# Optimization experiments

Measured on AMD Instinct MI355X. Metric: run time of the kernel, lower is better.

## Reference

```python
import jax, jax.numpy as jnp
import numpy as np
import math

H = 2048          # hidden_size
NH = 16           # num_attn_heads
HD = H // NH      # attn head dim = 128
NFW = 4           # num_lact_heads
FD = H // NFW     # fw head dim = 512
DH = FD           # inter_multi = 1.0
CHUNK = 512       # lact_chunk_size
WINDOW = 2048     # window_size
ROPE_BASE = 500000.0
BASE_LR_INV = math.log(math.expm1(0.001))  # inv_softplus(1e-3)


def rmsnorm(x, w, eps=1e-6):
    return x * jax.lax.rsqrt(jnp.mean(x * x, axis=-1, keepdims=True) + eps) * w


def l2norm(x, eps=1e-12):
    return x * jax.lax.rsqrt(jnp.sum(x * x, axis=-1, keepdims=True) + eps)


def rope(x):  # x: [b, h, s, d], half-split convention
    d = x.shape[-1]
    s = x.shape[2]
    inv = 1.0 / (ROPE_BASE ** (jnp.arange(d // 2, dtype=jnp.float32) / (d // 2)))
    f = jnp.arange(s, dtype=jnp.float32)[:, None] * inv[None, :]  # [s, d/2]
    cos, sin = jnp.cos(f), jnp.sin(f)
    x1, x2 = x[..., : d // 2], x[..., d // 2:]
    return jnp.concatenate([x1 * cos - x2 * sin, x2 * cos + x1 * sin], axis=-1)


def setup_inputs() -> dict:
    key = jax.random.key(0)
    ks = jax.random.split(key, 8)
    b, s = 2, 2048
    return {
        "hidden_states": jax.random.normal(ks[0], (b, s, H), jnp.float32),
        "qkv_w": jax.random.normal(ks[1], (3 * H, H), jnp.float32) / math.sqrt(H),
        "q_norm_w": jnp.ones((H,), jnp.float32),
        "k_norm_w": jnp.ones((H,), jnp.float32),
        "qk_scale": jnp.ones((H, 2), jnp.float32),
        "qk_offset": jnp.zeros((H, 2), jnp.float32),
        "lr_w": jax.random.normal(ks[2], (3 * NFW, H), jnp.float32) / math.sqrt(H),
        "lr_b": jnp.zeros((3 * NFW,), jnp.float32),
        "w0": jax.random.normal(ks[3], (NFW, DH, FD), jnp.float32) / math.sqrt(FD),
        "w1": jax.random.normal(ks[4], (NFW, FD, DH), jnp.float32) / math.sqrt(DH),
        "w2": jax.random.normal(ks[5], (NFW, DH, FD), jnp.float32) / math.sqrt(FD),
        "ttt_norm_w": jnp.ones((FD,), jnp.float32),
        "o_proj_w": jax.random.normal(ks[6], (H, H), jnp.float32) / math.sqrt(H),
    }


def reference(hidden_states, qkv_w, q_norm_w, k_norm_w, qk_scale, qk_offset,
              lr_w, lr_b, w0, w1, w2, ttt_norm_w, o_proj_w):
    x = hidden_states
    b, s, _ = x.shape
    nc = s // CHUNK

    qkv = x @ qkv_w.T
    q, k, v = jnp.split(qkv, 3, axis=-1)
    q = rmsnorm(q, q_norm_w)
    k = rmsnorm(k, k_norm_w)

    # ---- TTT (fast-weight SwiGLU) branch ----
    fq = jax.nn.silu(q * qk_scale[:, 0] + qk_offset[:, 0])
    fk = jax.nn.silu(k * qk_scale[:, 1] + qk_offset[:, 1])
    fv = jax.nn.silu(v)
    tohead = lambda t: t.reshape(b, s, NFW, FD).transpose(0, 2, 1, 3)  # [b,h,s,d]
    fq, fk, fv = l2norm(tohead(fq)), l2norm(tohead(fk)), tohead(fv)

    lr = jax.nn.softplus(x @ lr_w.T + lr_b + BASE_LR_INV)          # [b,s,3*NFW]
    lr = lr.reshape(b, s, 3, NFW).transpose(2, 0, 3, 1)[..., None]  # [3,b,h,s,1]
    lr0, lr1, lr2 = lr[0], lr[1], lr[2]

    chunkify = lambda t: t.reshape(b, NFW, nc, CHUNK, -1).transpose(2, 0, 1, 3, 4)
    qs, ks_, vs = chunkify(fq), chunkify(fk), chunkify(fv)
    l0s, l1s, l2s = chunkify(lr0), chunkify(lr1), chunkify(lr2)

    w0b = jnp.broadcast_to(w0, (b,) + w0.shape)
    w1b = jnp.broadcast_to(w1, (b,) + w1.shape)
    w2b = jnp.broadcast_to(w2, (b,) + w2.shape)

    def step(carry, xs):
        w0c, w1c, w2c = carry
        qc, kc, vc, l0, l1, l2 = xs
        # apply current fast weights to queries (strictly causal across chunks)
        hq = jax.nn.silu(jnp.einsum('bhcd,bhed->bhce', qc, w0c)) * \
             jnp.einsum('bhcd,bhed->bhce', qc, w2c)
        oc = jnp.einsum('bhce,bhde->bhcd', hq, w1c)
        # gradient-descent update on dot-product loss -sum(v * f(k))
        g1 = jnp.einsum('bhcd,bhed->bhce', kc, w0c)
        g2 = jnp.einsum('bhcd,bhed->bhce', kc, w2c)
        gate = jax.nn.silu(g1)
        hidden = gate * g2
        dhidden = jnp.einsum('bhcd,bhde->bhce', vc, w1c)  # w1^T v
        dh2 = dhidden * gate
        sig = jax.nn.sigmoid(g1)
        dh1 = dhidden * g2 * (sig * (1.0 + g1 * (1.0 - sig)))  # silu'(g1)
        w1n = w1c + jnp.einsum('bhcd,bhce->bhde', l1 * vc, hidden)
        w0n = w0c + jnp.einsum('bhce,bhcd->bhed', l0 * dh1, kc)
        w2n = w2c + jnp.einsum('bhce,bhcd->bhed', l2 * dh2, kc)
        return (w0n, w1n, w2n), oc

    _, o_chunks = jax.lax.scan(step, (w0b, w1b, w2b), (qs, ks_, vs, l0s, l1s, l2s))
    o_ttt = o_chunks.transpose(1, 2, 0, 3, 4).reshape(b, NFW, s, FD)
    o_ttt = rmsnorm(o_ttt, ttt_norm_w)
    o_ttt = o_ttt.transpose(0, 2, 1, 3).reshape(b, s, H)

    # ---- sliding-window attention branch ----
    qa = rope(q.reshape(b, s, NH, HD).transpose(0, 2, 1, 3))
    ka = rope(k.reshape(b, s, NH, HD).transpose(0, 2, 1, 3))
    va = v.reshape(b, s, NH, HD).transpose(0, 2, 1, 3)
    scores = jnp.einsum('bhqd,bhkd->bhqk', qa, ka) / math.sqrt(HD)
    i = jnp.arange(s)
    mask = (i[:, None] >= i[None, :]) & (i[:, None] - i[None, :] < WINDOW)
    scores = jnp.where(mask, scores, jnp.float32(-1e9))
    p = jax.nn.softmax(scores, axis=-1)
    attn = jnp.einsum('bhqk,bhkd->bhqd', p, va).transpose(0, 2, 1, 3).reshape(b, s, H)

    return (attn + o_ttt) @ o_proj_w.T
```

## Files before the change

### kernel.cpp

```cpp
#include <hip/hip_runtime.h>
#include <hip/hip_bf16.h>
#include <math.h>

using bf16 = __hip_bfloat16;

namespace {

constexpr int cH = 2048;
constexpr int cNH = 16;
constexpr int cHD = 128;
constexpr int cNFW = 4;
constexpr int cFD = 512;
constexpr int cS = 2048;
constexpr float cRSQRT_HD = 0.08838834764831845f;
constexpr long ZL_ = 262144;
constexpr long ZG_ = 1048576;

typedef __attribute__((ext_vector_type(8))) short short8;
typedef __attribute__((ext_vector_type(4))) float f32x4;

__device__ __forceinline__ float sigmoidf_(float x) { return 1.0f / (1.0f + __expf(-x)); }
__device__ __forceinline__ float b2f(bf16 v) { return __bfloat162float(v); }
__device__ __forceinline__ bf16 f2b(float v) { return __float2bfloat16(v); }
__device__ __forceinline__ unsigned short f2bu(float f) {
  return __builtin_bit_cast(unsigned short, __float2bfloat16(f));
}

#if defined(__has_builtin)
#if __has_builtin(__builtin_amdgcn_global_load_lds)
#define HAVE_GLOAD 1
#endif
#endif

__device__ __forceinline__ void gload16(const bf16* g, short* ldsbase) {
#ifdef HAVE_GLOAD
  __builtin_amdgcn_global_load_lds((const __attribute__((address_space(1))) void*)g,
                                   (__attribute__((address_space(3))) void*)ldsbase, 16, 0, 0);
#else
  const int l = threadIdx.x & 63;
  *(uint4*)(ldsbase + l * 8) = *(const uint4*)g;
#endif
}

__device__ __forceinline__ void stage16(const bf16* src, short* dst) {
  *(uint4*)dst = *(const uint4*)src;
  *(uint4*)(dst + 8) = *(const uint4*)(src + 8);
}

__device__ __forceinline__ void store1(float* p, float v) { *p = v; }
__device__ __forceinline__ void store1(bf16* p, float v) { *p = f2b(v); }

template <int AMODE, int BMODE>
__device__ __forceinline__ void mm_core(const bf16* __restrict__ Ab, int lda,
                                        const bf16* __restrict__ Bb, int ldb, int K,
                                        const float* __restrict__ sc,
                                        short* As, short* Bs, f32x4 acc[4][4]) {
  const int t = threadIdx.x, lane = t & 63, g = lane >> 4, c16 = lane & 15;
  const int wv = t >> 6, wm = (wv >> 1) * 64, wn = (wv & 1) * 64;
  for (int k0 = 0; k0 < K; k0 += 32) {
    __syncthreads();
    if constexpr (AMODE == 0) {
      const int ch = wv * 2;
      const bf16* g0 = Ab + (size_t)(ch * 16 + (lane >> 2)) * lda + k0 + (lane & 3) * 8;
      gload16(g0, &As[ch * 512]);
      gload16(g0 + (size_t)16 * lda, &As[ch * 512 + 512]);
    } else {
      const int kk = t >> 3, mseg = (t & 7) * 16;
      const float s = sc[k0 + kk];
      const bf16* p = Ab + (size_t)(k0 + kk) * lda + mseg;
#pragma unroll
      for (int i = 0; i < 16; ++i) As[(mseg + i) * 32 + kk] = (short)f2bu(b2f(p[i]) * s);
    }
    if constexpr (BMODE == 0) {
      const int ch = wv * 2;
      const bf16* g0 = Bb + (size_t)(ch * 16 + (lane >> 2)) * ldb + k0 + (lane & 3) * 8;
      gload16(g0, &Bs[ch * 512]);
      gload16(g0 + (size_t)16 * ldb, &Bs[ch * 512 + 512]);
    } else {
      const int kk = t >> 3, cseg = (t & 7) * 16;
      const short* p = (const short*)(Bb + (size_t)(k0 + kk) * ldb + cseg);
#pragma unroll
      for (int i = 0; i < 16; ++i) Bs[(cseg + i) * 32 + kk] = p[i];
    }
    __syncthreads();
    short8 af[4], bfr[4];
#pragma unroll
    for (int mi = 0; mi < 4; ++mi) af[mi] = *(const short8*)&As[(wm + mi * 16 + c16) * 32 + g * 8];
#pragma unroll
    for (int ni = 0; ni < 4; ++ni) bfr[ni] = *(const short8*)&Bs[(wn + ni * 16 + c16) * 32 + g * 8];
#pragma unroll
    for (int mi = 0; mi < 4; ++mi)
#pragma unroll
      for (int ni = 0; ni < 4; ++ni)
        acc[mi][ni] = __builtin_amdgcn_mfma_f32_16x16x32_bf16(af[mi], bfr[ni], acc[mi][ni], 0, 0, 0);
  }
}

template <bool ACC, bool MIR, typename TC>
__device__ __forceinline__ void mm_store(TC* Cb, bf16* Mb, int ldc, int rb, int cb, f32x4 acc[4][4]) {
  const int t = threadIdx.x, lane = t & 63, g = lane >> 4, c16 = lane & 15;
  const int wv = t >> 6, wm = (wv >> 1) * 64, wn = (wv & 1) * 64;
  const int rbase = rb + wm, cbase = cb + wn;
#pragma unroll
  for (int mi = 0; mi < 4; ++mi)
#pragma unroll
    for (int ni = 0; ni < 4; ++ni) {
      const int col = cbase + ni * 16 + c16;
#pragma unroll
      for (int r = 0; r < 4; ++r) {
        const int row = rbase + mi * 16 + g * 4 + r;
        TC* cp = Cb + (size_t)row * ldc + col;
        if constexpr (ACC) {
          float nv = *cp + acc[mi][ni][r];
          *cp = nv;
          if constexpr (MIR) Mb[(size_t)row * ldc + col] = f2b(nv);
        } else {
          store1(cp, acc[mi][ni][r]);
        }
      }
    }
}

template <typename TC, int BMODE>
__global__ __launch_bounds__(256) void k_mm(const bf16* __restrict__ A, int lda, long zsa,
                                            const bf16* __restrict__ B, int ldb, long zsb,
                                            TC* __restrict__ C, int ldc, long zsc, int K) {
  __shared__ short As[128 * 32];
  __shared__ short Bs[128 * 32];
  const int z = blockIdx.z;
  const bf16* Ab = A + (size_t)z * zsa + (size_t)blockIdx.y * 128 * lda;
  const bf16* Bb = (BMODE == 0) ? (B + (size_t)z * zsb + (size_t)blockIdx.x * 128 * ldb)
                                : (B + (size_t)z * zsb + blockIdx.x * 128);
  f32x4 acc[4][4];
  const f32x4 zero4 = {0.f, 0.f, 0.f, 0.f};
#pragma unroll
  for (int i = 0; i < 4; ++i)
#pragma unroll
    for (int j = 0; j < 4; ++j) acc[i][j] = zero4;
  mm_core<0, BMODE>(Ab, lda, Bb, ldb, K, nullptr, As, Bs, acc);
  mm_store<false, false>(C + (size_t)z * zsc, (bf16*)nullptr, ldc, blockIdx.y * 128, blockIdx.x * 128, acc);
}

__global__ __launch_bounds__(256) void k_fuse1(const bf16* __restrict__ fq, const bf16* __restrict__ fk,
                                               const bf16* __restrict__ fv,
                                               const bf16* __restrict__ w0b, const bf16* __restrict__ w1bc,
                                               const bf16* __restrict__ w2b,
                                               bf16* __restrict__ hq, bf16* __restrict__ trH,
                                               bf16* __restrict__ trD1, bf16* __restrict__ trD2,
                                               bf16* __restrict__ trK, bf16* __restrict__ trV,
                                               const float* __restrict__ lr0, const float* __restrict__ lr1,
                                               const float* __restrict__ lr2,
                                               const bf16* __restrict__ occPrev,
                                               const float* __restrict__ tw, bf16* __restrict__ y,
                                               int chunk) {
  __shared__ short S[12288];
  __shared__ float red[4];
  const int id = blockIdx.x, t = threadIdx.x;
  const size_t choff = (size_t)chunk * 262144;

  if (id < 512) {
    const int bh = id >> 6, tile = id & 63, by = tile >> 3, bx = tile & 7;
    const int lane = t & 63, g = lane >> 4, c16 = lane & 15, wv = t >> 6;
    const int wm = (wv >> 1) * 32, wn = (wv & 1) * 32;
    const bf16* Aq = fq + (size_t)bh * ZG_ + choff + (size_t)(by * 64) * cFD;
    const bf16* Ak = fk + (size_t)bh * ZG_ + choff + (size_t)(by * 64) * cFD;
    const bf16* Av = fv + (size_t)bh * ZG_ + choff + (size_t)(by * 64) * cFD;
    const bf16* B0 = w0b + (size_t)bh * ZL_ + (size_t)(bx * 64) * cFD;
    const bf16* B2 = w2b + (size_t)bh * ZL_ + (size_t)(bx * 64) * cFD;
    const bf16* B1 = w1bc + (size_t)bh * ZL_ + bx * 64;

    f32x4 acc[5][2][2];
    const f32x4 zero4 = {0.f, 0.f, 0.f, 0.f};
#pragma unroll
    for (int v = 0; v < 5; ++v)
#pragma unroll
      for (int i = 0; i < 2; ++i)
#pragma unroll
        for (int j = 0; j < 2; ++j) acc[v][i][j] = zero4;

    const int srow = wv * 16 + (lane >> 2), scol = (lane & 3) * 8;
    for (int k0 = 0; k0 < 512; k0 += 32) {
      __syncthreads();
      gload16(Aq + (size_t)srow * cFD + k0 + scol, &S[0 + wv * 512]);
      gload16(Ak + (size_t)srow * cFD + k0 + scol, &S[2048 + wv * 512]);
      gload16(Av + (size_t)srow * cFD + k0 + scol, &S[4096 + wv * 512]);
      gload16(B0 + (size_t)srow * cFD + k0 + scol, &S[6144 + wv * 512]);
      gload16(B2 + (size_t)srow * cFD + k0 + scol, &S[8192 + wv * 512]);
      {
        const int kk = t >> 3, e8 = (t & 7) * 8;
        const short* p = (const short*)(B1 + (size_t)(k0 + kk) * cFD + e8);
#pragma unroll
        for (int i = 0; i < 8; ++i) S[10240 + (e8 + i) * 32 + kk] = p[i];
      }
      __syncthreads();
      short8 aq[2], ak[2], av[2], b0[2], b2[2], b1[2];
#pragma unroll
      for (int mi = 0; mi < 2; ++mi) {
        const int ro = (wm + mi * 16 + c16) * 32 + g * 8;
        aq[mi] = *(const short8*)&S[0 + ro];
        ak[mi] = *(const short8*)&S[2048 + ro];
        av[mi] = *(const short8*)&S[4096 + ro];
      }
#pragma unroll
      for (int ni = 0; ni < 2; ++ni) {
        const int ro = (wn + ni * 16 + c16) * 32 + g * 8;
        b0[ni] = *(const short8*)&S[6144 + ro];
        b2[ni] = *(const short8*)&S[8192 + ro];
        b1[ni] = *(const short8*)&S[10240 + ro];
      }
#pragma unroll
      for (int mi = 0; mi < 2; ++mi)
#pragma unroll
        for (int ni = 0; ni < 2; ++ni) {
          acc[0][mi][ni] = __builtin_amdgcn_mfma_f32_16x16x32_bf16(aq[mi], b0[ni], acc[0][mi][ni], 0, 0, 0);
          acc[1][mi][ni] = __builtin_amdgcn_mfma_f32_16x16x32_bf16(aq[mi], b2[ni], acc[1][mi][ni], 0, 0, 0);
          acc[2][mi][ni] = __builtin_amdgcn_mfma_f32_16x16x32_bf16(ak[mi], b0[ni], acc[2][mi][ni], 0, 0, 0);
          acc[3][mi][ni] = __builtin_amdgcn_mfma_f32_16x16x32_bf16(ak[mi], b2[ni], acc[3][mi][ni], 0, 0, 0);
          acc[4][mi][ni] = __builtin_amdgcn_mfma_f32_16x16x32_bf16(av[mi], b1[ni], acc[4][mi][ni], 0, 0, 0);
        }
    }

    float l0v[2][4], l2v[2][4];
#pragma unroll
    for (int mi = 0; mi < 2; ++mi)
#pragma unroll
      for (int r = 0; r < 4; ++r) {
        const int row = by * 64 + wm + mi * 16 + g * 4 + r;
        l0v[mi][r] = lr0[bh * 2048 + chunk * 512 + row];
        l2v[mi][r] = lr2[bh * 2048 + chunk * 512 + row];
      }
#pragma unroll
    for (int mi = 0; mi < 2; ++mi)
#pragma unroll
      for (int ni = 0; ni < 2; ++ni)
#pragma unroll
        for (int r = 0; r < 4; ++r) {
          float hq1 = acc[0][mi][ni][r], hq2 = acc[1][mi][ni][r];
          float g1 = acc[2][mi][ni][r], g2 = acc[3][mi][ni][r], dh = acc[4][mi][ni][r];
          acc[0][mi][ni][r] = hq1 * sigmoidf_(hq1) * hq2;
          float sg = sigmoidf_(g1);
          float gate = g1 * sg;
          acc[1][mi][ni][r] = gate * g2;
          acc[2][mi][ni][r] = l0v[mi][r] * dh * g2 * (sg * (1.0f + g1 * (1.0f - sg)));
          acc[3][mi][ni][r] = l2v[mi][r] * dh * gate;
        }

    short* Ts = S;
    bf16* dst0 = hq + (size_t)bh * ZL_;
    bf16* dstT[3] = {trH + (size_t)bh * ZL_, trD1 + (size_t)bh * ZL_, trD2 + (size_t)bh * ZL_};
#pragma unroll
    for (int rd = 0; rd < 4; ++rd) {
      __syncthreads();
#pragma unroll
      for (int mi = 0; mi < 2; ++mi)
#pragma unroll
        for (int ni = 0; ni < 2; ++ni)
#pragma unroll
          for (int r = 0; r < 4; ++r) {
            const int row = wm + mi * 16 + g * 4 + r, col = wn + ni * 16 + c16;
            if (rd == 0) Ts[row * 66 + col] = (short)f2bu(acc[0][mi][ni][r]);
            else Ts[col * 66 + row] = (short)f2bu(acc[rd][mi][ni][r]);
          }
      __syncthreads();
      const int rr = t >> 2, cs = (t & 3) * 16;
      unsigned short u[16] __attribute__((aligned(16)));
#pragma unroll
      for (int i = 0; i < 16; ++i) u[i] = (unsigned short)Ts[rr * 66 + cs + i];
      bf16* dp = (rd == 0) ? (dst0 + (size_t)(by * 64 + rr) * cFD + bx * 64 + cs)
                           : (dstT[rd - 1] + (size_t)(bx * 64 + rr) * cFD + by * 64 + cs);
      *(uint4*)dp = *(uint4*)u;
      *(uint4*)(dp + 8) = *(uint4*)(u + 8);
    }
  } else if (id < 1536) {
    short* Ts = S;
    const int id2 = id - 512;
    const int var = id2 >> 9, bh = (id2 >> 6) & 7, by = (id2 >> 3) & 7, bx = id2 & 7;
    const bf16* src = ((var == 0) ? fk : fv) + choff + (size_t)bh * ZG_;
    bf16* dst = ((var == 0) ? trK : trV) + (size_t)bh * ZL_;
    {
      const int rr = t >> 2, cseg = (t & 3) * 16;
      if (var == 0) {
        stage16(src + (size_t)(by * 64 + rr) * cFD + bx * 64 + cseg, &Ts[rr * 72 + cseg]);
      } else {
        const float s = lr1[bh * 2048 + chunk * 512 + by * 64 + rr];
        const bf16* p = src + (size_t)(by * 64 + rr) * cFD + bx * 64 + cseg;
        unsigned short u[16] __attribute__((aligned(16)));
#pragma unroll
        for (int i = 0; i < 16; ++i) u[i] = f2bu(b2f(p[i]) * s);
        *(uint4*)&Ts[rr * 72 + cseg] = *(uint4*)u;
        *(uint4*)&Ts[rr * 72 + cseg + 8] = *(uint4*)(u + 8);
      }
    }
    __syncthreads();
    {
      const int oc_ = t >> 2, rseg = (t & 3) * 16;
      unsigned short u[16] __attribute__((aligned(16)));
#pragma unroll
      for (int i = 0; i < 16; ++i) u[i] = (unsigned short)Ts[(rseg + i) * 72 + oc_];
      bf16* dp = dst + (size_t)(bx * 64 + oc_) * cFD + by * 64 + rseg;
      *(uint4*)dp = *(uint4*)u;
      *(uint4*)(dp + 8) = *(uint4*)(u + 8);
    }
  } else {
    const int rrow = id - 1536;
    const int bh = rrow >> 9, rr = rrow & 511;
    const bf16* src = occPrev + ((size_t)bh * 512 + rr) * 512;
    float v0 = b2f(src[t]), v1 = b2f(src[t + 256]);
    float ss = v0 * v0 + v1 * v1;
    for (int d = 32; d; d >>= 1) ss += __shfl_down(ss, d);
    if ((t & 63) == 0) red[t >> 6] = ss;
    __syncthreads();
    const float rstd = rsqrtf((red[0] + red[1] + red[2] + red[3]) / cFD + 1e-6f);
    const int si = (chunk - 1) * 512 + rr;
    bf16* dst = y + ((size_t)((bh >> 2) * cS) + si) * cH + (bh & 3) * cFD;
    dst[t] = f2b(b2f(dst[t]) + v0 * rstd * tw[t]);
    dst[t + 256] = f2b(b2f(dst[t + 256]) + v1 * rstd * tw[t + 256]);
  }
}

__global__ __launch_bounds__(256) void k_updna(const bf16* __restrict__ trV, const bf16* __restrict__ trH,
                                               const bf16* __restrict__ trD1, const bf16* __restrict__ trD2,
                                               const bf16* __restrict__ trK,
                                               const bf16* __restrict__ hq, const bf16* __restrict__ w1bc,
                                               float* w0s, float* w1s, float* w2s,
                                               bf16* w0b, bf16* w1bn, bf16* w2b,
                                               bf16* __restrict__ occCur) {
  __shared__ short Sh[8192];
  const int id = blockIdx.x, t = threadIdx.x;
  if (id < 384) {
    short* As = Sh;
    short* Bs = Sh + 4096;
    const int z = id >> 4, tile = id & 15, by = tile >> 2, bx = tile & 3;
    const int var = z >> 3, bh = z & 7;
    const bf16 *Aa, *Bb;
    float* W;
    bf16* M;
    if (var == 0) {
      Aa = trV + (size_t)bh * ZL_ + (size_t)by * 128 * cFD;
      Bb = trH + (size_t)bh * ZL_ + (size_t)bx * 128 * cFD;
      W = w1s + (size_t)bh * ZL_; M = w1bn + (size_t)bh * ZL_;
    } else if (var == 1) {
      Aa = trD1 + (size_t)bh * ZL_ + (size_t)by * 128 * cFD;
      Bb = trK + (size_t)bh * ZL_ + (size_t)bx * 128 * cFD;
      W = w0s + (size_t)bh * ZL_; M = w0b + (size_t)bh * ZL_;
    } else {
      Aa = trD2 + (size_t)bh * ZL_ + (size_t)by * 128 * cFD;
      Bb = trK + (size_t)bh * ZL_ + (size_t)bx * 128 * cFD;
      W = w2s + (size_t)bh * ZL_; M = w2b + (size_t)bh * ZL_;
    }
    f32x4 acc[4][4];
    const f32x4 zero4 = {0.f, 0.f, 0.f, 0.f};
#pragma unroll
    for (int i = 0; i < 4; ++i)
#pragma unroll
      for (int j = 0; j < 4; ++j) acc[i][j] = zero4;
    mm_core<0, 0>(Aa, cFD, Bb, cFD, cFD, nullptr, As, Bs, acc);
    mm_store<true, true>(W, M, cFD, by * 128, bx * 128, acc);
  } else {
    const int id2 = id - 384;
    const int bh = id2 >> 6, tile = id2 & 63, by = tile >> 3, bx = tile & 7;
    const int lane = t & 63, g = lane >> 4, c16 = lane & 15, wv = t >> 6;
    const int wm = (wv >> 1) * 32, wn = (wv & 1) * 32;
    const bf16* Aa = hq + (size_t)bh * ZL_ + (size_t)(by * 64) * cFD;
    const bf16* Bb = w1bc + (size_t)bh * ZL_ + (size_t)(bx * 64) * cFD;
    short* As = Sh;
    short* Bs = Sh + 2048;
    f32x4 acc[2][2];
    const f32x4 zero4 = {0.f, 0.f, 0.f, 0.f};
#pragma unroll
    for (int i = 0; i < 2; ++i)
#pragma unroll
      for (int j = 0; j < 2; ++j) acc[i][j] = zero4;
    for (int k0 = 0; k0 < 512; k0 += 32) {
      __syncthreads();
      {
        const int srow = wv * 16 + (lane >> 2), scol = (lane & 3) * 8;
        gload16(Aa + (size_t)srow * cFD + k0 + scol, &As[wv * 512]);
        gload16(Bb + (size_t)srow * cFD + k0 + scol, &Bs[wv * 512]);
      }
      __syncthreads();
      short8 af[2], bfr[2];
#pragma unroll
      for (int mi = 0; mi < 2; ++mi) af[mi] = *(const short8*)&As[(wm + mi * 16 + c16) * 32 + g * 8];
#pragma unroll
      for (int ni = 0; ni < 2; ++ni) bfr[ni] = *(const short8*)&Bs[(wn + ni * 16 + c16) * 32 + g * 8];
#pragma unroll
      for (int mi = 0; mi < 2; ++mi)
#pragma unroll
        for (int ni = 0; ni < 2; ++ni)
          acc[mi][ni] = __builtin_amdgcn_mfma_f32_16x16x32_bf16(af[mi], bfr[ni], acc[mi][ni], 0, 0, 0);
    }
    bf16* C = occCur + (size_t)bh * ZL_;
#pragma unroll
    for (int mi = 0; mi < 2; ++mi)
#pragma unroll
      for (int ni = 0; ni < 2; ++ni) {
        const int col = bx * 64 + wn + ni * 16 + c16;
#pragma unroll
        for (int r = 0; r < 4; ++r) {
          const int row = by * 64 + wm + mi * 16 + g * 4 + r;
          C[(size_t)row * cFD + col] = f2b(acc[mi][ni][r]);
        }
      }
  }
}

__global__ __launch_bounds__(256) void k_norm(const bf16* __restrict__ occ,
                                              const float* __restrict__ tw, bf16* __restrict__ y,
                                              int chunk) {
  __shared__ float red[4];
  const int rrow = blockIdx.x;
  const int bh = rrow >> 9, rr = rrow & 511;
  const int t = threadIdx.x;
  const bf16* src = occ + ((size_t)bh * 512 + rr) * 512;
  float v0 = b2f(src[t]), v1 = b2f(src[t + 256]);
  float ss = v0 * v0 + v1 * v1;
  for (int d = 32; d; d >>= 1) ss += __shfl_down(ss, d);
  if ((t & 63) == 0) red[t >> 6] = ss;
  __syncthreads();
  const float rstd = rsqrtf((red[0] + red[1] + red[2] + red[3]) / cFD + 1e-6f);
  const int si = chunk * 512 + rr;
  bf16* dst = y + ((size_t)((bh >> 2) * cS) + si) * cH + (bh & 3) * cFD;
  dst[t] = f2b(b2f(dst[t]) + v0 * rstd * tw[t]);
  dst[t + 256] = f2b(b2f(dst[t + 256]) + v1 * rstd * tw[t + 256]);
}

__global__ __launch_bounds__(256) void k_cvt(const float* __restrict__ src, bf16* __restrict__ dst) {
  const size_t i = ((size_t)blockIdx.x * 256 + threadIdx.x) * 8;
  float4 a = *(const float4*)(src + i), b = *(const float4*)(src + i + 4);
  unsigned short u[8] __attribute__((aligned(16)));
  u[0] = f2bu(a.x); u[1] = f2bu(a.y); u[2] = f2bu(a.z); u[3] = f2bu(a.w);
  u[4] = f2bu(b.x); u[5] = f2bu(b.y); u[6] = f2bu(b.z); u[7] = f2bu(b.w);
  *(uint4*)(dst + i) = *(uint4*)u;
}

__global__ __launch_bounds__(256) void k_winit(const float* __restrict__ w0, const float* __restrict__ w1,
                                               const float* __restrict__ w2,
                                               float* __restrict__ w0s, float* __restrict__ w1s,
                                               float* __restrict__ w2s) {
  const size_t i = (size_t)blockIdx.x * 256 + threadIdx.x;
  const int bh = (int)(i >> 18);
  const int f = bh & 3;
  const size_t off = i & 262143;
  const float* src; float* dst;
  if (blockIdx.y == 0) { src = w0; dst = w0s; }
  else if (blockIdx.y == 1) { src = w1; dst = w1s; }
  else { src = w2; dst = w2s; }
  dst[i] = src[(size_t)f * 262144 + off];
}

__global__ __launch_bounds__(64) void k_rope_tab(float* __restrict__ ct, float* __restrict__ stb) {
  const int si = blockIdx.x, j = threadIdx.x;
  float inv = powf(500000.0f, -(float)j / 64.0f);
  float ang = (float)si * inv;
  ct[(size_t)si * 64 + j] = cosf(ang);
  stb[(size_t)si * 64 + j] = sinf(ang);
}

__global__ __launch_bounds__(256) void k_lr(const float* __restrict__ x, const float* __restrict__ lr_w,
                                            const float* __restrict__ lr_b,
                                            float* lr0, float* lr1, float* lr2, float base) {
  const int token = blockIdx.x, b_ = token >> 11, si = token & 2047;
  const int wv = threadIdx.x >> 6, lane = threadIdx.x & 63;
  const float* xr = x + (size_t)token * cH;
#pragma unroll
  for (int jj = 0; jj < 3; ++jj) {
    const int j = wv * 3 + jj;
    const float* wr = lr_w + (size_t)j * cH;
    float s = 0.f;
    for (int k = lane; k < cH; k += 64) s += xr[k] * wr[k];
    for (int d = 32; d; d >>= 1) s += __shfl_down(s, d);
    if (lane == 0) {
      float v = s + lr_b[j] + base;
      float sp = (v > 15.f) ? v : log1pf(expf(v));
      const int tt = j >> 2, f = j & 3;
      float* dst = (tt == 0 ? lr0 : tt == 1 ? lr1 : lr2);
      dst[(size_t)(b_ * cNFW + f) * cS + si] = sp;
    }
  }
}

__global__ __launch_bounds__(256) void k_normrope(bf16* __restrict__ qkvh,
                                                  const float* __restrict__ qnw, const float* __restrict__ knw,
                                                  const float* __restrict__ ct, const float* __restrict__ stb,
                                                  bf16* __restrict__ qa, bf16* __restrict__ ka) {
  const int token = blockIdx.x, b_ = token >> 11, si = token & 2047;
  const int t = threadIdx.x;
  __shared__ float buf[cH];
  __shared__ float red[4];
  bf16* base = qkvh + (size_t)token * 3 * cH;
  for (int pass = 0; pass < 2; ++pass) {
    __syncthreads();
    bf16* src = base + pass * cH;
    const float* nw = pass ? knw : qnw;
    float ss = 0.f;
    for (int i = t; i < cH; i += 256) {
      float v = b2f(src[i]);
      buf[i] = v;
      ss += v * v;
    }
    for (int d = 32; d; d >>= 1) ss += __shfl_down(ss, d);
    if ((t & 63) == 0) red[t >> 6] = ss;
    __syncthreads();
    const float rstd = rsqrtf((red[0] + red[1] + red[2] + red[3]) / cH + 1e-6f);
    for (int i = t; i < cH; i += 256) {
      float v = buf[i] * rstd * nw[i];
      buf[i] = v;
      src[i] = f2b(v);
    }
    __syncthreads();
    bf16* dst = pass ? ka : qa;
    const float scale = pass ? 1.f : cRSQRT_HD;
    const int hh = t >> 4, j0 = (t & 15) * 4;
    const float* cr = ct + (size_t)si * 64 + j0;
    const float* sr = stb + (size_t)si * 64 + j0;
    bf16* drow = dst + ((size_t)(b_ * cNH + hh) * cS + si) * cHD;
    unsigned short u1[4] __attribute__((aligned(8))), u2[4] __attribute__((aligned(8)));
#pragma unroll
    for (int i = 0; i < 4; ++i) {
      float x1 = buf[hh * cHD + j0 + i], x2 = buf[hh * cHD + 64 + j0 + i];
      u1[i] = f2bu((x1 * cr[i] - x2 * sr[i]) * scale);
      u2[i] = f2bu((x2 * cr[i] + x1 * sr[i]) * scale);
    }
    *(uint2*)(drow + j0) = *(uint2*)u1;
    *(uint2*)(drow + 64 + j0) = *(uint2*)u2;
  }
}

__global__ __launch_bounds__(256) void k_vtr(const bf16* __restrict__ qkvh, bf16* __restrict__ vt) {
  const int tile = blockIdx.x, h = blockIdx.y, b_ = blockIdx.z;
  __shared__ short Ts[64 * 136];
  const int t = threadIdx.x;
  {
    const int r = t >> 2, seg = (t & 3) * 32;
    const bf16* src = qkvh + ((size_t)(b_ * cS) + tile * 64 + r) * 3 * cH + 2 * cH + h * cHD + seg;
    stage16(src, &Ts[r * 136 + seg]);
    stage16(src + 16, &Ts[r * 136 + seg + 16]);
  }
  __syncthreads();
  {
    const int d = t >> 1, seg2 = (t & 1) * 32;
    unsigned short u[32] __attribute__((aligned(16)));
#pragma unroll
    for (int i = 0; i < 32; ++i) u[i] = (unsigned short)Ts[(seg2 + i) * 136 + d];
    bf16* dp = vt + ((size_t)(b_ * cNH + h) * cHD + d) * cS + tile * 64 + seg2;
    *(uint4*)dp = *(uint4*)u;
    *(uint4*)(dp + 8) = *(uint4*)(u + 8);
    *(uint4*)(dp + 16) = *(uint4*)(u + 16);
    *(uint4*)(dp + 24) = *(uint4*)(u + 24);
  }
}

__global__ __launch_bounds__(256) void k_fqkv(const bf16* __restrict__ qkvh,
                                              const float* __restrict__ qk_scale,
                                              const float* __restrict__ qk_offset,
                                              bf16* fq, bf16* fk, bf16* fv) {
  const int token = blockIdx.x, b_ = token >> 11, si = token & 2047;
  const int t = threadIdx.x;
  const bf16* base = qkvh + (size_t)token * 3 * cH;
#pragma unroll
  for (int pass = 0; pass < 2; ++pass) {
    const bf16* src = base + pass * cH;
    bf16* fdst = pass ? fk : fq;
    const int head = t >> 6, lane = t & 63;
    float f[8];
    float ss2 = 0.f;
#pragma unroll
    for (int k = 0; k < 8; ++k) {
      const int idx = head * cFD + lane + k * 64;
      float v = b2f(src[idx]);
      float u = v * qk_scale[idx * 2 + pass] + qk_offset[idx * 2 + pass];
      float fv_ = u * sigmoidf_(u);
      f[k] = fv_;
      ss2 += fv_ * fv_;
    }
    for (int d = 1; d < 64; d <<= 1) ss2 += __shfl_xor(ss2, d);
    const float sc2 = rsqrtf(ss2 + 1e-12f);
    bf16* dst = fdst + ((size_t)(b_ * cNFW + head) * cS + si) * cFD;
#pragma unroll
    for (int k = 0; k < 8; ++k) dst[lane + k * 64] = f2b(f[k] * sc2);
  }
  const bf16* vr = base + 2 * cH;
  for (int i = t; i < cH; i += 256) {
    float v = b2f(vr[i]);
    fv[((size_t)(b_ * cNFW + (i >> 9)) * cS + si) * cFD + (i & 511)] = f2b(v * sigmoidf_(v));
  }
}

__global__ __launch_bounds__(256) void k_attn5(const bf16* __restrict__ qa, const bf16* __restrict__ ka,
                                               const bf16* __restrict__ vt, bf16* __restrict__ y) {
  const int id = blockIdx.x;
  const int xcd = id & 7;
  const int j = id >> 3;
  const int p = j & 15;
  const int hb = (j >> 4) * 8 + xcd;
  const int h = hb & 15, b_ = hb >> 4;
  __shared__ short Ks[64 * 136];
  __shared__ short Vts[128 * 72];
  const int t = threadIdx.x, lane = t & 63, g = lane >> 4, c16 = lane & 15, wv = t >> 6;
  const size_t hbq = (size_t)(b_ * cNH + h) * cS;
  const bf16* vb = vt + (size_t)(b_ * cNH + h) * (size_t)(cHD * cS);
  const int r = t >> 2, seg = (t & 3) * 32;
  const int dv = t >> 1, seg2 = (t & 1) * 32;
  const f32x4 zero4 = {0.f, 0.f, 0.f, 0.f};

  for (int half = 0; half < 2; ++half) {
    const int qt = half ? p : 31 - p;
    const int q0 = qt * 64;
    short8 qf[4];
    {
      const bf16* qsrc = qa + (hbq + q0 + wv * 16 + c16) * cHD;
#pragma unroll
      for (int ks = 0; ks < 4; ++ks) qf[ks] = *(const short8*)(qsrc + ks * 32 + g * 8);
    }
    f32x4 o[8];
#pragma unroll
    for (int i = 0; i < 8; ++i) o[i] = zero4;
    float m[4], l[4];
#pragma unroll
    for (int rr = 0; rr < 4; ++rr) { m[rr] = -1e30f; l[rr] = 0.f; }

    uint4 kp0, kp1, kp2, kp3, vp0, vp1, vp2, vp3;
    {
      const bf16* ksrc = ka + (hbq + r) * cHD + seg;
      kp0 = *(const uint4*)ksrc; kp1 = *(const uint4*)(ksrc + 8);
      kp2 = *(const uint4*)(ksrc + 16); kp3 = *(const uint4*)(ksrc + 24);
      const bf16* vsrc = vb + (size_t)dv * cS + seg2;
      vp0 = *(const uint4*)vsrc; vp1 = *(const uint4*)(vsrc + 8);
      vp2 = *(const uint4*)(vsrc + 16); vp3 = *(const uint4*)(vsrc + 24);
    }

    for (int kt = 0; kt <= qt; ++kt) {
      __syncthreads();
      {
        short* kd = &Ks[r * 136 + seg];
        *(uint4*)kd = kp0; *(uint4*)(kd + 8) = kp1;
        *(uint4*)(kd + 16) = kp2; *(uint4*)(kd + 24) = kp3;
        short* vd = &Vts[dv * 72 + seg2];
        *(uint4*)vd = vp0; *(uint4*)(vd + 8) = vp1;
        *(uint4*)(vd + 16) = vp2; *(uint4*)(vd + 24) = vp3;
      }
      __syncthreads();
      if (kt < qt) {
        const bf16* ksrc = ka + (hbq + (kt + 1) * 64 + r) * cHD + seg;
        kp0 = *(const uint4*)ksrc; kp1 = *(const uint4*)(ksrc + 8);
        kp2 = *(const uint4*)(ksrc + 16); kp3 = *(const uint4*)(ksrc + 24);
        const bf16* vsrc = vb + (size_t)dv * cS + (kt + 1) * 64 + seg2;
        vp0 = *(const uint4*)vsrc; vp1 = *(const uint4*)(vsrc + 8);
        vp2 = *(const uint4*)(vsrc + 16); vp3 = *(const uint4*)(vsrc + 24);
      } else if (half == 0) {
        const bf16* ksrc = ka + (hbq + r) * cHD + seg;
        kp0 = *(const uint4*)ksrc; kp1 = *(const uint4*)(ksrc + 8);
        kp2 = *(const uint4*)(ksrc + 16); kp3 = *(const uint4*)(ksrc + 24);
        const bf16* vsrc = vb + (size_t)dv * cS + seg2;
        vp0 = *(const uint4*)vsrc; vp1 = *(const uint4*)(vsrc + 8);
        vp2 = *(const uint4*)(vsrc + 16); vp3 = *(const uint4*)(vsrc + 24);
      }

      f32x4 s4[4];
#pragma unroll
      for (int ni = 0; ni < 4; ++ni) s4[ni] = zero4;
      __builtin_amdgcn_s_setprio(1);
#pragma unroll
      for (int ks = 0; ks < 4; ++ks) {
#pragma unroll
        for (int ni = 0; ni < 4; ++ni) {
          short8 bb = *(const short8*)&Ks[(ni * 16 + c16) * 136 + ks * 32 + g * 8];
          s4[ni] = __builtin_amdgcn_mfma_f32_16x16x32_bf16(qf[ks], bb, s4[ni], 0, 0, 0);
        }
      }
      __builtin_amdgcn_s_setprio(0);
      __syncthreads();
      if (kt == qt) {
#pragma unroll
        for (int ni = 0; ni < 4; ++ni) {
          const int kv = kt * 64 + ni * 16 + c16;
#pragma unroll
          for (int rr = 0; rr < 4; ++rr) {
            const int qr = q0 + wv * 16 + g * 4 + rr;
            if (kv > qr) s4[ni][rr] = -1e9f;
          }
        }
      }
      float mx[4];
#pragma unroll
      for (int rr = 0; rr < 4; ++rr)
        mx[rr] = fmaxf(fmaxf(s4[0][rr], s4[1][rr]), fmaxf(s4[2][rr], s4[3][rr]));
#pragma unroll
      for (int d = 1; d < 16; d <<= 1)
#pragma unroll
        for (int rr = 0; rr < 4; ++rr) mx[rr] = fmaxf(mx[rr], __shfl_xor(mx[rr], d));
      bool need = false;
#pragma unroll
      for (int rr = 0; rr < 4; ++rr) need |= (mx[rr] > m[rr] + 8.f);
      if (__any(need)) {
        float corr[4];
#pragma unroll
        for (int rr = 0; rr < 4; ++rr) {
          float mn = fmaxf(m[rr], mx[rr]);
          corr[rr] = __expf(m[rr] - mn);
          m[rr] = mn;
        }
#pragma unroll
        for (int rr = 0; rr < 4; ++rr) l[rr] *= corr[rr];
#pragma unroll
        for (int nf = 0; nf < 8; ++nf)
#pragma unroll
          for (int rr = 0; rr < 4; ++rr) o[nf][rr] *= corr[rr];
      }
      float psum[4] = {0.f, 0.f, 0.f, 0.f};
#pragma unroll
      for (int ni = 0; ni < 4; ++ni)
#pragma unroll
        for (int rr = 0; rr < 4; ++rr) {
          float pp = __expf(s4[ni][rr] - m[rr]);
          s4[ni][rr] = pp;
          psum[rr] += pp;
        }
#pragma unroll
      for (int d = 1; d < 16; d <<= 1)
#pragma unroll
        for (int rr = 0; rr < 4; ++rr) psum[rr] += __shfl_xor(psum[rr], d);
#pragma unroll
      for (int rr = 0; rr < 4; ++rr) l[rr] += psum[rr];
      short* pw = &Ks[wv * 1152];
#pragma unroll
      for (int ni = 0; ni < 4; ++ni)
#pragma unroll
        for (int rr = 0; rr < 4; ++rr)
          pw[(g * 4 + rr) * 72 + ni * 16 + c16] = (short)f2bu(s4[ni][rr]);
      __builtin_amdgcn_s_setprio(1);
#pragma unroll
      for (int ks2 = 0; ks2 < 2; ++ks2) {
        short8 a = *(const short8*)&pw[c16 * 72 + ks2 * 32 + g * 8];
#pragma unroll
        for (int nf = 0; nf < 8; ++nf) {
          short8 bb = *(const short8*)&Vts[(nf * 16 + c16) * 72 + ks2 * 32 + g * 8];
          o[nf] = __builtin_amdgcn_mfma_f32_16x16x32_bf16(a, bb, o[nf], 0, 0, 0);
        }
      }
      __builtin_amdgcn_s_setprio(0);
    }
    float inv[4];
#pragma unroll
    for (int rr = 0; rr < 4; ++rr) inv[rr] = 1.f / l[rr];
#pragma unroll
    for (int nf = 0; nf < 8; ++nf)
#pragma unroll
      for (int rr = 0; rr < 4; ++rr) {
        const size_t row = (size_t)(b_ * cS) + q0 + wv * 16 + g * 4 + rr;
        y[row * cH + h * cHD + nf * 16 + c16] = f2b(o[nf][rr] * inv[rr]);
      }
  }
}

}

extern "C" void kernel_launch(void* const* d_in, const int* in_sizes, int n_in,
                              void* d_out, int out_size, void* d_ws, size_t ws_size,
                              hipStream_t stream) {
  (void)in_sizes; (void)n_in; (void)out_size; (void)ws_size;
  const float* x         = (const float*)d_in[0];
  const float* qkv_w     = (const float*)d_in[1];
  const float* q_norm_w  = (const float*)d_in[2];
  const float* k_norm_w  = (const float*)d_in[3];
  const float* qk_scale  = (const float*)d_in[4];
  const float* qk_offset = (const float*)d_in[5];
  const float* lr_w      = (const float*)d_in[6];
  const float* lr_b      = (const float*)d_in[7];
  const float* w0        = (const float*)d_in[8];
  const float* w1        = (const float*)d_in[9];
  const float* w2        = (const float*)d_in[10];
  const float* ttt_nw    = (const float*)d_in[11];
  const float* o_proj_w  = (const float*)d_in[12];
  float* out = (float*)d_out;

  char* Wb = (char*)d_ws;
  bf16* qkvh = (bf16*)Wb;
  bf16* hq   = (bf16*)(Wb + 0UL);
  bf16* trH  = (bf16*)(Wb + 4194304UL);
  bf16* trD1 = (bf16*)(Wb + 8388608UL);
  bf16* trD2 = (bf16*)(Wb + 12582912UL);
  bf16* trK  = (bf16*)(Wb + 16777216UL);
  bf16* trV  = (bf16*)(Wb + 20971520UL);
  bf16* occA = (bf16*)(Wb + 25165824UL);
  bf16* occB = (bf16*)(Wb + 29360128UL);
  bf16* w0b  = (bf16*)(Wb + 33554432UL);
  bf16* w1b0 = (bf16*)(Wb + 37748736UL);
  bf16* w2b  = (bf16*)(Wb + 41943040UL);
  bf16* w1b1 = (bf16*)(Wb + 46137344UL);
  bf16* opwb = (bf16*)(Wb + 0UL);
  size_t off = 50331648UL;
  bf16* fqb = (bf16*)(Wb + off); off += 16777216UL;
  bf16* fkb = (bf16*)(Wb + off); off += 16777216UL;
  bf16* fvb = (bf16*)(Wb + off); off += 16777216UL;
  float* w0s = (float*)(Wb + off); off += 8388608UL;
  float* w1s = (float*)(Wb + off); off += 8388608UL;
  float* w2s = (float*)(Wb + off); off += 8388608UL;
  float* lr0 = (float*)(Wb + off); off += 65536UL;
  float* lr1 = (float*)(Wb + off); off += 65536UL;
  float* lr2 = (float*)(Wb + off); off += 65536UL;
  bf16* y = (bf16*)(Wb + off); off += 16777216UL;
  float* ct  = (float*)(Wb + off); off += 524288UL;
  float* stb = (float*)(Wb + off); off += 524288UL;
  bf16* xb = fqb;
  bf16* qkvwb = fkb;
  bf16* qa = fqb;
  bf16* ka = fkb;
  bf16* vt = fvb;
  bf16* w1m[2] = {w1b0, w1b1};
  bf16* occb[2] = {occA, occB};

  const float base_lr_inv = logf(expm1f(0.001f));
  dim3 blk(256);

  k_winit<<<dim3(8192, 3), blk, 0, stream>>>(w0, w1, w2, w0s, w1s, w2s);
  k_rope_tab<<<dim3(2048), dim3(64), 0, stream>>>(ct, stb);
  k_cvt<<<dim3(4096), blk, 0, stream>>>(x, xb);
  k_cvt<<<dim3(6144), blk, 0, stream>>>(qkv_w, qkvwb);
  k_mm<bf16, 0><<<dim3(48, 32, 1), blk, 0, stream>>>(xb, 2048, 0, qkvwb, 2048, 0, qkvh, 6144, 0, 2048);
  k_lr<<<dim3(4096), blk, 0, stream>>>(x, lr_w, lr_b, lr0, lr1, lr2, base_lr_inv);
  k_normrope<<<dim3(4096), blk, 0, stream>>>(qkvh, q_norm_w, k_norm_w, ct, stb, qa, ka);
  k_vtr<<<dim3(32, 16, 2), blk, 0, stream>>>(qkvh, vt);
  k_attn5<<<dim3(512), blk, 0, stream>>>(qa, ka, vt, y);
  k_fqkv<<<dim3(4096), blk, 0, stream>>>(qkvh, qk_scale, qk_offset, fqb, fkb, fvb);
  k_cvt<<<dim3(3072), blk, 0, stream>>>(w0s, w0b);

  for (int c = 0; c < 4; ++c) {
    const int g1 = (c == 0) ? 1536 : 5632;
    k_fuse1<<<dim3(g1), blk, 0, stream>>>(fqb, fkb, fvb, w0b, w1m[c & 1], w2b,
                                          hq, trH, trD1, trD2, trK, trV,
                                          lr0, lr1, lr2,
                                          (c == 0) ? occb[0] : occb[(c - 1) & 1],
                                          ttt_nw, y, c);
    k_updna<<<dim3(896), blk, 0, stream>>>(trV, trH, trD1, trD2, trK, hq, w1m[c & 1],
                                           w0s, w1s, w2s, w0b, w1m[(c + 1) & 1], w2b,
                                           occb[c & 1]);
  }
  k_norm<<<dim3(4096), blk, 0, stream>>>(occb[1], ttt_nw, y, 3);
  k_cvt<<<dim3(2048), blk, 0, stream>>>(o_proj_w, opwb);
  k_mm<float, 0><<<dim3(16, 32, 1), blk, 0, stream>>>(y, 2048, 0, opwb, 2048, 0, out, 2048, 0, 2048);
}
```

Before: 743.5 us.

## Merge prep kernels, widen attention tiles to 128 queries, vectorize W1 transpose

```diff
diff --git a/kernel.cpp b/kernel.cpp
--- a/kernel.cpp
+++ b/kernel.cpp
@@ -153,7 +153,7 @@
                                                const bf16* __restrict__ occPrev,
                                                const float* __restrict__ tw, bf16* __restrict__ y,
                                                int chunk) {
-  __shared__ short S[12288];
+  __shared__ short S[12800];
   __shared__ float red[4];
   const int id = blockIdx.x, t = threadIdx.x;
   const size_t choff = (size_t)chunk * 262144;
@@ -187,10 +187,12 @@
       gload16(B0 + (size_t)srow * cFD + k0 + scol, &S[6144 + wv * 512]);
       gload16(B2 + (size_t)srow * cFD + k0 + scol, &S[8192 + wv * 512]);
       {
-        const int kk = t >> 3, e8 = (t & 7) * 8;
-        const short* p = (const short*)(B1 + (size_t)(k0 + kk) * cFD + e8);
-#pragma unroll
-        for (int i = 0; i < 8; ++i) S[10240 + (e8 + i) * 32 + kk] = p[i];
+        const int e = t & 63, kg = t >> 6;
+        unsigned short u[8] __attribute__((aligned(16)));
+#pragma unroll
+        for (int i = 0; i < 8; ++i)
+          u[i] = *(const unsigned short*)(B1 + (size_t)(k0 + kg * 8 + i) * cFD + e);
+        *(uint4*)&S[10240 + e * 40 + kg * 8] = *(uint4*)u;
       }
       __syncthreads();
       short8 aq[2], ak[2], av[2], b0[2], b2[2], b1[2];
@@ -206,7 +208,7 @@
         const int ro = (wn + ni * 16 + c16) * 32 + g * 8;
         b0[ni] = *(const short8*)&S[6144 + ro];
         b2[ni] = *(const short8*)&S[8192 + ro];
-        b1[ni] = *(const short8*)&S[10240 + ro];
+        b1[ni] = *(const short8*)&S[10240 + (wn + ni * 16 + c16) * 40 + g * 8];
       }
 #pragma unroll
       for (int mi = 0; mi < 2; ++mi)
@@ -405,24 +407,33 @@
   }
 }
 
-__global__ __launch_bounds__(256) void k_norm(const bf16* __restrict__ occ,
-                                              const float* __restrict__ tw, bf16* __restrict__ y,
-                                              int chunk) {
+__global__ __launch_bounds__(256) void k_normcvt(const bf16* __restrict__ occ,
+                                                 const float* __restrict__ tw, bf16* __restrict__ y,
+                                                 const float* __restrict__ opw, bf16* __restrict__ opwb,
+                                                 int chunk) {
   __shared__ float red[4];
-  const int rrow = blockIdx.x;
-  const int bh = rrow >> 9, rr = rrow & 511;
-  const int t = threadIdx.x;
-  const bf16* src = occ + ((size_t)bh * 512 + rr) * 512;
-  float v0 = b2f(src[t]), v1 = b2f(src[t + 256]);
-  float ss = v0 * v0 + v1 * v1;
-  for (int d = 32; d; d >>= 1) ss += __shfl_down(ss, d);
-  if ((t & 63) == 0) red[t >> 6] = ss;
-  __syncthreads();
-  const float rstd = rsqrtf((red[0] + red[1] + red[2] + red[3]) / cFD + 1e-6f);
-  const int si = chunk * 512 + rr;
-  bf16* dst = y + ((size_t)((bh >> 2) * cS) + si) * cH + (bh & 3) * cFD;
-  dst[t] = f2b(b2f(dst[t]) + v0 * rstd * tw[t]);
-  dst[t + 256] = f2b(b2f(dst[t + 256]) + v1 * rstd * tw[t + 256]);
+  const int id = blockIdx.x, t = threadIdx.x;
+  if (id < 4096) {
+    const int bh = id >> 9, rr = id & 511;
+    const bf16* src = occ + ((size_t)bh * 512 + rr) * 512;
+    float v0 = b2f(src[t]), v1 = b2f(src[t + 256]);
+    float ss = v0 * v0 + v1 * v1;
+    for (int d = 32; d; d >>= 1) ss += __shfl_down(ss, d);
+    if ((t & 63) == 0) red[t >> 6] = ss;
+    __syncthreads();
+    const float rstd = rsqrtf((red[0] + red[1] + red[2] + red[3]) / cFD + 1e-6f);
+    const int si = chunk * 512 + rr;
+    bf16* dst = y + ((size_t)((bh >> 2) * cS) + si) * cH + (bh & 3) * cFD;
+    dst[t] = f2b(b2f(dst[t]) + v0 * rstd * tw[t]);
+    dst[t + 256] = f2b(b2f(dst[t + 256]) + v1 * rstd * tw[t + 256]);
+  } else {
+    const size_t i = ((size_t)(id - 4096) * 256 + t) * 8;
+    float4 a = *(const float4*)(opw + i), b = *(const float4*)(opw + i + 4);
+    unsigned short u[8] __attribute__((aligned(16)));
+    u[0] = f2bu(a.x); u[1] = f2bu(a.y); u[2] = f2bu(a.z); u[3] = f2bu(a.w);
+    u[4] = f2bu(b.x); u[5] = f2bu(b.y); u[6] = f2bu(b.z); u[7] = f2bu(b.w);
+    *(uint4*)(opwb + i) = *(uint4*)u;
+  }
 }
 
 __global__ __launch_bounds__(256) void k_cvt(const float* __restrict__ src, bf16* __restrict__ dst) {
@@ -434,48 +445,64 @@
   *(uint4*)(dst + i) = *(uint4*)u;
 }
 
-__global__ __launch_bounds__(256) void k_winit(const float* __restrict__ w0, const float* __restrict__ w1,
-                                               const float* __restrict__ w2,
-                                               float* __restrict__ w0s, float* __restrict__ w1s,
-                                               float* __restrict__ w2s) {
-  const size_t i = (size_t)blockIdx.x * 256 + threadIdx.x;
-  const int bh = (int)(i >> 18);
-  const int f = bh & 3;
-  const size_t off = i & 262143;
-  const float* src; float* dst;
-  if (blockIdx.y == 0) { src = w0; dst = w0s; }
-  else if (blockIdx.y == 1) { src = w1; dst = w1s; }
-  else { src = w2; dst = w2s; }
-  dst[i] = src[(size_t)f * 262144 + off];
-}
-
-__global__ __launch_bounds__(64) void k_rope_tab(float* __restrict__ ct, float* __restrict__ stb) {
-  const int si = blockIdx.x, j = threadIdx.x;
-  float inv = powf(500000.0f, -(float)j / 64.0f);
-  float ang = (float)si * inv;
-  ct[(size_t)si * 64 + j] = cosf(ang);
-  stb[(size_t)si * 64 + j] = sinf(ang);
-}
-
-__global__ __launch_bounds__(256) void k_lr(const float* __restrict__ x, const float* __restrict__ lr_w,
-                                            const float* __restrict__ lr_b,
-                                            float* lr0, float* lr1, float* lr2, float base) {
-  const int token = blockIdx.x, b_ = token >> 11, si = token & 2047;
-  const int wv = threadIdx.x >> 6, lane = threadIdx.x & 63;
-  const float* xr = x + (size_t)token * cH;
-#pragma unroll
-  for (int jj = 0; jj < 3; ++jj) {
-    const int j = wv * 3 + jj;
-    const float* wr = lr_w + (size_t)j * cH;
-    float s = 0.f;
-    for (int k = lane; k < cH; k += 64) s += xr[k] * wr[k];
-    for (int d = 32; d; d >>= 1) s += __shfl_down(s, d);
-    if (lane == 0) {
-      float v = s + lr_b[j] + base;
-      float sp = (v > 15.f) ? v : log1pf(expf(v));
-      const int tt = j >> 2, f = j & 3;
-      float* dst = (tt == 0 ? lr0 : tt == 1 ? lr1 : lr2);
-      dst[(size_t)(b_ * cNFW + f) * cS + si] = sp;
+__global__ __launch_bounds__(256) void k_prep(const float* __restrict__ x, const float* __restrict__ qkv_w,
+                                              const float* __restrict__ w0, const float* __restrict__ w1,
+                                              const float* __restrict__ w2,
+                                              const float* __restrict__ lr_w, const float* __restrict__ lr_b,
+                                              bf16* __restrict__ xb, bf16* __restrict__ qkvwb,
+                                              float* __restrict__ w0s, float* __restrict__ w1s,
+                                              float* __restrict__ w2s,
+                                              float* __restrict__ ct, float* __restrict__ stb,
+                                              float* lr0, float* lr1, float* lr2, float base) {
+  const int id = blockIdx.x, t = threadIdx.x;
+  if (id < 4096) {
+    const size_t i = ((size_t)id * 256 + t) * 8;
+    float4 a = *(const float4*)(x + i), b = *(const float4*)(x + i + 4);
+    unsigned short u[8] __attribute__((aligned(16)));
+    u[0] = f2bu(a.x); u[1] = f2bu(a.y); u[2] = f2bu(a.z); u[3] = f2bu(a.w);
+    u[4] = f2bu(b.x); u[5] = f2bu(b.y); u[6] = f2bu(b.z); u[7] = f2bu(b.w);
+    *(uint4*)(xb + i) = *(uint4*)u;
+  } else if (id < 10240) {
+    const size_t i = ((size_t)(id - 4096) * 256 + t) * 8;
+    float4 a = *(const float4*)(qkv_w + i), b = *(const float4*)(qkv_w + i + 4);
+    unsigned short u[8] __attribute__((aligned(16)));
+    u[0] = f2bu(a.x); u[1] = f2bu(a.y); u[2] = f2bu(a.z); u[3] = f2bu(a.w);
+    u[4] = f2bu(b.x); u[5] = f2bu(b.y); u[6] = f2bu(b.z); u[7] = f2bu(b.w);
+    *(uint4*)(qkvwb + i) = *(uint4*)u;
+  } else if (id < 16384) {
+    const int sub = id - 10240;
+    const int w = sub >> 11, blk = sub & 2047;
+    const size_t i = ((size_t)blk * 256 + t) * 4;
+    const int f = (int)((i >> 18) & 3);
+    const size_t off = i & 262143;
+    const float* src = (w == 0) ? w0 : (w == 1) ? w1 : w2;
+    float* dst = (w == 0) ? w0s : (w == 1) ? w1s : w2s;
+    *(float4*)(dst + i) = *(const float4*)(src + (size_t)f * 262144 + off);
+  } else if (id < 16896) {
+    const int gid = (id - 16384) * 256 + t;
+    const int si = gid >> 6, jj = gid & 63;
+    float inv = powf(500000.0f, -(float)jj / 64.0f);
+    float ang = (float)si * inv;
+    ct[(size_t)si * 64 + jj] = cosf(ang);
+    stb[(size_t)si * 64 + jj] = sinf(ang);
+  } else {
+    const int token = id - 16896, b_ = token >> 11, si = token & 2047;
+    const int wv = t >> 6, lane = t & 63;
+    const float* xr = x + (size_t)token * cH;
+#pragma unroll
+    for (int jj = 0; jj < 3; ++jj) {
+      const int j = wv * 3 + jj;
+      const float* wr = lr_w + (size_t)j * cH;
+      float s = 0.f;
+      for (int k = lane; k < cH; k += 64) s += xr[k] * wr[k];
+      for (int d = 32; d; d >>= 1) s += __shfl_down(s, d);
+      if (lane == 0) {
+        float v = s + lr_b[j] + base;
+        float sp = (v > 15.f) ? v : log1pf(expf(v));
+        const int tt = j >> 2, f = j & 3;
+        float* dst = (tt == 0 ? lr0 : tt == 1 ? lr1 : lr2);
+        dst[(size_t)(b_ * cNFW + f) * cS + si] = sp;
+      }
     }
   }
 }
@@ -587,26 +614,27 @@
   }
 }
 
-__global__ __launch_bounds__(256) void k_attn5(const bf16* __restrict__ qa, const bf16* __restrict__ ka,
+__global__ __launch_bounds__(512) void k_attn6(const bf16* __restrict__ qa, const bf16* __restrict__ ka,
                                                const bf16* __restrict__ vt, bf16* __restrict__ y) {
   const int id = blockIdx.x;
   const int xcd = id & 7;
   const int j = id >> 3;
-  const int p = j & 15;
-  const int hb = (j >> 4) * 8 + xcd;
+  const int p = j & 7;
+  const int hb = (j >> 3) * 8 + xcd;
   const int h = hb & 15, b_ = hb >> 4;
-  __shared__ short Ks[64 * 136];
+  __shared__ short KsP[9216];
   __shared__ short Vts[128 * 72];
   const int t = threadIdx.x, lane = t & 63, g = lane >> 4, c16 = lane & 15, wv = t >> 6;
   const size_t hbq = (size_t)(b_ * cNH + h) * cS;
   const bf16* vb = vt + (size_t)(b_ * cNH + h) * (size_t)(cHD * cS);
-  const int r = t >> 2, seg = (t & 3) * 32;
-  const int dv = t >> 1, seg2 = (t & 1) * 32;
+  const int r = t >> 3, seg = (t & 7) * 16;
+  const int dv = t >> 2, seg2 = (t & 3) * 16;
   const f32x4 zero4 = {0.f, 0.f, 0.f, 0.f};
 
   for (int half = 0; half < 2; ++half) {
-    const int qt = half ? p : 31 - p;
-    const int q0 = qt * 64;
+    const int qt = half ? p : 15 - p;
+    const int q0 = qt * 128;
+    const int nkt = 2 * qt + 2;
     short8 qf[4];
     {
       const bf16* qsrc = qa + (hbq + q0 + wv * 16 + c16) * cHD;
@@ -620,41 +648,33 @@
 #pragma unroll
     for (int rr = 0; rr < 4; ++rr) { m[rr] = -1e30f; l[rr] = 0.f; }
 
-    uint4 kp0, kp1, kp2, kp3, vp0, vp1, vp2, vp3;
+    uint4 kp0, kp1, vp0, vp1;
     {
       const bf16* ksrc = ka + (hbq + r) * cHD + seg;
       kp0 = *(const uint4*)ksrc; kp1 = *(const uint4*)(ksrc + 8);
-      kp2 = *(const uint4*)(ksrc + 16); kp3 = *(const uint4*)(ksrc + 24);
       const bf16* vsrc = vb + (size_t)dv * cS + seg2;
       vp0 = *(const uint4*)vsrc; vp1 = *(const uint4*)(vsrc + 8);
-      vp2 = *(const uint4*)(vsrc + 16); vp3 = *(const uint4*)(vsrc + 24);
-    }
-
-    for (int kt = 0; kt <= qt; ++kt) {
+    }
+
+    for (int kt = 0; kt < nkt; ++kt) {
       __syncthreads();
       {
-        short* kd = &Ks[r * 136 + seg];
+        short* kd = &KsP[r * 136 + seg];
         *(uint4*)kd = kp0; *(uint4*)(kd + 8) = kp1;
-        *(uint4*)(kd + 16) = kp2; *(uint4*)(kd + 24) = kp3;
         short* vd = &Vts[dv * 72 + seg2];
         *(uint4*)vd = vp0; *(uint4*)(vd + 8) = vp1;
-        *(uint4*)(vd + 16) = vp2; *(uint4*)(vd + 24) = vp3;
       }
       __syncthreads();
-      if (kt < qt) {
+      if (kt + 1 < nkt) {
         const bf16* ksrc = ka + (hbq + (kt + 1) * 64 + r) * cHD + seg;
         kp0 = *(const uint4*)ksrc; kp1 = *(const uint4*)(ksrc + 8);
-        kp2 = *(const uint4*)(ksrc + 16); kp3 = *(const uint4*)(ksrc + 24);
         const bf16* vsrc = vb + (size_t)dv * cS + (kt + 1) * 64 + seg2;
         vp0 = *(const uint4*)vsrc; vp1 = *(const uint4*)(vsrc + 8);
-        vp2 = *(const uint4*)(vsrc + 16); vp3 = *(const uint4*)(vsrc + 24);
       } else if (half == 0) {
         const bf16* ksrc = ka + (hbq + r) * cHD + seg;
         kp0 = *(const uint4*)ksrc; kp1 = *(const uint4*)(ksrc + 8);
-        kp2 = *(const uint4*)(ksrc + 16); kp3 = *(const uint4*)(ksrc + 24);
         const bf16* vsrc = vb + (size_t)dv * cS + seg2;
         vp0 = *(const uint4*)vsrc; vp1 = *(const uint4*)(vsrc + 8);
-        vp2 = *(const uint4*)(vsrc + 16); vp3 = *(const uint4*)(vsrc + 24);
       }
 
       f32x4 s4[4];
@@ -665,13 +685,13 @@
       for (int ks = 0; ks < 4; ++ks) {
 #pragma unroll
         for (int ni = 0; ni < 4; ++ni) {
-          short8 bb = *(const short8*)&Ks[(ni * 16 + c16) * 136 + ks * 32 + g * 8];
+          short8 bb = *(const short8*)&KsP[(ni * 16 + c16) * 136 + ks * 32 + g * 8];
           s4[ni] = __builtin_amdgcn_mfma_f32_16x16x32_bf16(qf[ks], bb, s4[ni], 0, 0, 0);
         }
       }
       __builtin_amdgcn_s_setprio(0);
       __syncthreads();
-      if (kt == qt) {
+      if (kt * 64 + 64 > q0) {
 #pragma unroll
         for (int ni = 0; ni < 4; ++ni) {
           const int kv = kt * 64 + ni * 16 + c16;
@@ -723,7 +743,7 @@
         for (int rr = 0; rr < 4; ++rr) psum[rr] += __shfl_xor(psum[rr], d);
 #pragma unroll
       for (int rr = 0; rr < 4; ++rr) l[rr] += psum[rr];
-      short* pw = &Ks[wv * 1152];
+      short* pw = &KsP[wv * 1152];
 #pragma unroll
       for (int ni = 0; ni < 4; ++ni)
 #pragma unroll
@@ -814,15 +834,13 @@
   const float base_lr_inv = logf(expm1f(0.001f));
   dim3 blk(256);
 
-  k_winit<<<dim3(8192, 3), blk, 0, stream>>>(w0, w1, w2, w0s, w1s, w2s);
-  k_rope_tab<<<dim3(2048), dim3(64), 0, stream>>>(ct, stb);
-  k_cvt<<<dim3(4096), blk, 0, stream>>>(x, xb);
-  k_cvt<<<dim3(6144), blk, 0, stream>>>(qkv_w, qkvwb);
+  k_prep<<<dim3(20992), blk, 0, stream>>>(x, qkv_w, w0, w1, w2, lr_w, lr_b,
+                                          xb, qkvwb, w0s, w1s, w2s, ct, stb,
+                                          lr0, lr1, lr2, base_lr_inv);
   k_mm<bf16, 0><<<dim3(48, 32, 1), blk, 0, stream>>>(xb, 2048, 0, qkvwb, 2048, 0, qkvh, 6144, 0, 2048);
-  k_lr<<<dim3(4096), blk, 0, stream>>>(x, lr_w, lr_b, lr0, lr1, lr2, base_lr_inv);
   k_normrope<<<dim3(4096), blk, 0, stream>>>(qkvh, q_norm_w, k_norm_w, ct, stb, qa, ka);
   k_vtr<<<dim3(32, 16, 2), blk, 0, stream>>>(qkvh, vt);
-  k_attn5<<<dim3(512), blk, 0, stream>>>(qa, ka, vt, y);
+  k_attn6<<<dim3(256), dim3(512), 0, stream>>>(qa, ka, vt, y);
   k_fqkv<<<dim3(4096), blk, 0, stream>>>(qkvh, qk_scale, qk_offset, fqb, fkb, fvb);
   k_cvt<<<dim3(3072), blk, 0, stream>>>(w0s, w0b);
 
@@ -837,7 +855,6 @@
                                            w0s, w1s, w2s, w0b, w1m[(c + 1) & 1], w2b,
                                            occb[c & 1]);
   }
-  k_norm<<<dim3(4096), blk, 0, stream>>>(occb[1], ttt_nw, y, 3);
-  k_cvt<<<dim3(2048), blk, 0, stream>>>(o_proj_w, opwb);
+  k_normcvt<<<dim3(6144), blk, 0, stream>>>(occb[1], ttt_nw, y, o_proj_w, opwb, 3);
   k_mm<float, 0><<<dim3(16, 32, 1), blk, 0, stream>>>(y, 2048, 0, opwb, 2048, 0, out, 2048, 0, 2048);
 }
```

After: 726.3 us. 2.3% less time.
